# Kernel optimization log

Measured on AMD Instinct MI355X. Metric: run time of the kernel, lower is better.

Reference implementation:

```python
import jax, jax.numpy as jnp
import numpy as np

# neuralef_loss_cfg constants (kernel = '10nnn_sigm1.0')
T = 10.0        # cfg['t']
ALPHA = 0.05    # cfg['alpha']
KNN = 10        # parsed from '10nnn'
SIGMA2 = 1.0    # parsed from 'sigm1.0'
EPS = 1e-12     # F.normalize eps

N_TOKENS, D_FEAT, K_EIG = 8192, 768, 256


def setup_inputs() -> dict:
    key = jax.random.key(0)
    k1, k2 = jax.random.split(key)
    FF = jax.random.normal(k1, (N_TOKENS, D_FEAT), dtype=jnp.float32)
    Psi = jax.random.normal(k2, (N_TOKENS, K_EIG), dtype=jnp.float32)
    return {"FF": FF, "Psi": Psi}


def _gram_knn(FF):
    """torch.no_grad() block: RBF affinity -> topk KNN sparsify -> sym -> degree norm."""
    # input_l2_normalize: F.normalize(FF, dim=1)
    FFn = FF / jnp.maximum(jnp.linalg.norm(FF, axis=1, keepdims=True), EPS)
    sq = jnp.sum(FFn * FFn, axis=-1)                       # [N]
    # pairwise squared distances -> RBF kernel  [N, N]
    A = jnp.exp(-(sq[:, None] + sq[None, :] - 2.0 * (FFn @ FFn.T)) / (2.0 * SIGMA2))
    vals, idx = jax.lax.top_k(A, KNN)                      # [N, KNN]
    N = A.shape[0]
    rows = jnp.arange(N)
    # res.scatter_(1, idx, vals) on zeros_like(A)
    res = jnp.zeros_like(A).at[rows[:, None], idx].set(vals)
    gram = 0.5 * (res + res.T)
    gram = gram.at[rows, rows].set(0.0)                    # zero diagonal
    Dsum = jnp.sum(gram, axis=-1)
    # D = Dsum.rsqrt(); D[D==inf] = 0  (Dsum >= 0 always since vals >= 0)
    D = jnp.where(Dsum > 0, jax.lax.rsqrt(Dsum), 0.0)
    return D[:, None] * gram * D[None, :]


def reference(FF, Psi):
    N = Psi.shape[0]
    Psi = Psi * (T / N)
    gram = jax.lax.stop_gradient(_gram_knn(FF))            # [N, N]
    gPsi = gram @ Psi                                      # [N, K]
    R = Psi.T @ gPsi                                       # [K, K]
    # no_sg = False: R_hat = Psi.T.detach() @ gram @ Psi
    R_hat = jax.lax.stop_gradient(Psi).T @ gPsi
    loss = -jnp.trace(R)
    reg = jnp.sum(jnp.triu(R_hat ** 2, 1))
    return jnp.stack([loss, reg * ALPHA])
```

## Files before the change

### kernel.cpp

```cpp
#include <hip/hip_runtime.h>
#include <math.h>

#define N_TOK 8192
#define D_FEAT 768
#define K_EIG 256
#define KNN 10
#define CAP 256
#define NCHUNK 4
#define CHUNK 2048

typedef unsigned short ushort_t;
typedef float f32x4 __attribute__((ext_vector_type(4)));
typedef short bf16x8 __attribute__((ext_vector_type(8)));
typedef unsigned short u16x8 __attribute__((ext_vector_type(8)));
typedef unsigned short u16x4 __attribute__((ext_vector_type(4)));

__device__ inline float u2f(unsigned u) { union { unsigned u; float f; } c; c.u = u; return c.f; }
__device__ inline unsigned f2u(float f) { union { unsigned u; float f; } c; c.f = f; return c.u; }
__device__ inline ushort_t f2bf_rne(float f) {
  const unsigned u = f2u(f);
  return (ushort_t)((u + 0x7fffu + ((u >> 16) & 1u)) >> 16);
}
__device__ inline ushort_t f2key(float f) {
  const unsigned h = f2u(f) >> 16;
  return (ushort_t)((h & 0x8000u) ? (h ^ 0xFFFFu) : (h | 0x8000u));
}
__device__ inline float key2f(unsigned k) {
  const unsigned h = (k & 0x8000u) ? (k ^ 0x8000u) : (k ^ 0xFFFFu);
  return u2f(h << 16);
}
__device__ inline unsigned wave_max_u32(unsigned m) {
#pragma unroll
  for (int s = 1; s < 64; s <<= 1) m = max(m, (unsigned)__shfl_xor((int)m, s, 64));
  return m;
}

__global__ __launch_bounds__(192) void k_norm(const float* __restrict__ FF,
                                              ushort_t* __restrict__ FFbf,
                                              float* __restrict__ rn,
                                              float* __restrict__ sqv) {
  const int row = blockIdx.x;
  const int tid = threadIdx.x;
  const float4 v = *(const float4*)&FF[(size_t)row * D_FEAT + tid * 4];
  float s = v.x * v.x + v.y * v.y + v.z * v.z + v.w * v.w;
  __shared__ float red[3];
  for (int m = 32; m > 0; m >>= 1) s += __shfl_xor(s, m, 64);
  if ((tid & 63) == 0) red[tid >> 6] = s;
  __syncthreads();
  const float tot = red[0] + red[1] + red[2];
  const float scale = 1.f / fmaxf(sqrtf(tot), 1e-12f);
  float4 w;
  w.x = v.x * scale; w.y = v.y * scale; w.z = v.z * scale; w.w = v.w * scale;
  float s2 = w.x * w.x + w.y * w.y + w.z * w.z + w.w * w.w;
  u16x4 o;
  o[0] = f2bf_rne(w.x); o[1] = f2bf_rne(w.y); o[2] = f2bf_rne(w.z); o[3] = f2bf_rne(w.w);
  *(u16x4*)&FFbf[(size_t)row * D_FEAT + tid * 4] = o;
  for (int m = 32; m > 0; m >>= 1) s2 += __shfl_xor(s2, m, 64);
  __syncthreads();
  if ((tid & 63) == 0) red[tid >> 6] = s2;
  __syncthreads();
  if (tid == 0) { sqv[row] = red[0] + red[1] + red[2]; rn[row] = scale; }
}

#define AS1(p) ((const __attribute__((address_space(1))) void*)(p))
#define AS3(p) ((__attribute__((address_space(3))) void*)(p))

__global__ __launch_bounds__(256) void k_gemm(const ushort_t* __restrict__ FFbf,
                                              ushort_t* __restrict__ Cs,
                                              ushort_t* __restrict__ Gmax,
                                              int cbase) {
  __shared__ ushort_t smem[16384];
  const int tid = threadIdx.x;
  const int mb = blockIdx.x & 63;
  const int nb = blockIdx.x >> 6;
  const int rbase = mb * 128;
  const int cb = cbase + nb * 128;
  const int w = tid >> 6, lane = tid & 63;
  const int wr = w >> 1, wc = w & 1;
  const int fr = lane & 15;
  const int kg = lane >> 4;
  const int srow = tid >> 2, skq = tid & 3;

  f32x4 acc[4][4];
#pragma unroll
  for (int m = 0; m < 4; ++m)
#pragma unroll
    for (int n = 0; n < 4; ++n) acc[m][n] = (f32x4){0.f, 0.f, 0.f, 0.f};

#define STAGE(b, kt) do { \
    const ushort_t* ga = FFbf + (size_t)(rbase + srow) * D_FEAT + (kt) * 32 + skq * 8; \
    const ushort_t* gb = FFbf + (size_t)(cb + srow) * D_FEAT + (kt) * 32 + skq * 8; \
    char* abase = (char*)&smem[(b) * 4096]; \
    char* bbase = (char*)&smem[8192 + (b) * 4096]; \
    __builtin_amdgcn_global_load_lds(AS1(ga), AS3(abase + tid * 16), 16, 0, 0); \
    __builtin_amdgcn_global_load_lds(AS1(gb), AS3(bbase + tid * 16), 16, 0, 0); \
    __builtin_amdgcn_global_load_lds(AS1(ga + (size_t)64 * D_FEAT), AS3(abase + 4096 + tid * 16), 16, 0, 0); \
    __builtin_amdgcn_global_load_lds(AS1(gb + (size_t)64 * D_FEAT), AS3(bbase + 4096 + tid * 16), 16, 0, 0); \
  } while (0)

  STAGE(0, 0);
  int buf = 0;
  for (int kt = 0; kt < D_FEAT / 32; ++kt) {
    __syncthreads();
    if (kt + 1 < D_FEAT / 32) STAGE(buf ^ 1, kt + 1);
    bf16x8 af[4], bfr[4];
#pragma unroll
    for (int m = 0; m < 4; ++m)
      af[m] = *(const bf16x8*)&smem[buf * 4096 + (wr * 64 + m * 16 + fr) * 32 + kg * 8];
#pragma unroll
    for (int n = 0; n < 4; ++n)
      bfr[n] = *(const bf16x8*)&smem[8192 + buf * 4096 + (wc * 64 + n * 16 + fr) * 32 + kg * 8];
#pragma unroll
    for (int m = 0; m < 4; ++m)
#pragma unroll
      for (int n = 0; n < 4; ++n)
        acc[m][n] = __builtin_amdgcn_mfma_f32_16x16x32_bf16(af[m], bfr[n], acc[m][n], 0, 0, 0);
    buf ^= 1;
  }
#undef STAGE

  __syncthreads();
#pragma unroll
  for (int m = 0; m < 4; ++m)
#pragma unroll
    for (int n = 0; n < 4; ++n)
#pragma unroll
      for (int r = 0; r < 4; ++r)
        smem[(wr * 64 + m * 16 + kg * 4 + r) * 128 + wc * 64 + n * 16 + fr] = f2key(acc[m][n][r]);
  __syncthreads();
#pragma unroll
  for (int i = 0; i < 8; ++i) {
    const int off = i * 4096 + tid * 16;
    const int row = off >> 8;
    const int colb = off & 255;
    const u16x8 v = *(const u16x8*)((const char*)smem + off);
    *(u16x8*)((char*)Cs + (size_t)(rbase + row) * (CHUNK * 2) + (size_t)nb * 256 + colb) = v;
  }
  {
    const int r2 = tid >> 1;
    const int gh = (tid & 1) * 8;
    u16x8 gmv;
#pragma unroll
    for (int g = 0; g < 8; ++g) {
      const u16x8 grp = *(const u16x8*)&smem[r2 * 128 + (gh + g) * 8];
      unsigned mx = 0;
#pragma unroll
      for (int j = 0; j < 8; ++j) mx = max(mx, (unsigned)(ushort_t)grp[j]);
      gmv[g] = (ushort_t)mx;
    }
    *(u16x8*)&Gmax[(size_t)(rbase + r2) * 256 + nb * 16 + gh] = gmv;
  }
}

__global__ __launch_bounds__(256) void k_sel(const ushort_t* __restrict__ Cs,
                                             const ushort_t* __restrict__ Gmax,
                                             int chunk,
                                             float* __restrict__ pd, int* __restrict__ pi) {
  const int tid = threadIdx.x;
  const int lane = tid & 63;
  const int row = blockIdx.x * 4 + (tid >> 6);
  const ushort_t* src = Cs + (size_t)row * CHUNK;

  const u16x4 gm = *(const u16x4*)&Gmax[(size_t)row * 256 + lane * 4];
  unsigned cur[4];
#pragma unroll
  for (int k = 0; k < 4; ++k)
    cur[k] = (((unsigned)(ushort_t)gm[k]) << 16) | (unsigned)(lane * 4 + k);
  unsigned keep = 0;
#pragma unroll
  for (int r = 0; r < 16; ++r) {
    unsigned m = max(max(cur[0], cur[1]), max(cur[2], cur[3]));
    m = wave_max_u32(m);
    if (lane == r) keep = m;
    const unsigned gid = m & 0xFFu;
    if (lane == (int)(gid >> 2)) {
      const int sl = (int)(gid & 3u);
#pragma unroll
      for (int k = 0; k < 4; ++k)
        if (k == sl) cur[k] = 0;
    }
  }
  const unsigned gid2 = keep & 0xFFu;
  unsigned E[8];
  if (lane < 16) {
    const u16x8 g = *(const u16x8*)&src[gid2 * 8];
#pragma unroll
    for (int j = 0; j < 8; ++j)
      E[j] = (((unsigned)(ushort_t)g[j]) << 16) | (gid2 * 8 + (unsigned)j);
  } else {
#pragma unroll
    for (int j = 0; j < 8; ++j) E[j] = 0;
  }
  unsigned keep2 = 0;
#pragma unroll
  for (int r = 0; r < 16; ++r) {
    unsigned m = E[0];
#pragma unroll
    for (int j = 1; j < 8; ++j) m = max(m, E[j]);
    m = wave_max_u32(m);
    if (lane == r) keep2 = m;
    const unsigned col = m & 0xFFFFu;
    const bool mine = (lane < 16) && ((col >> 3) == gid2);
    const int sl = (int)(col & 7u);
#pragma unroll
    for (int j = 0; j < 8; ++j)
      if (mine && j == sl) E[j] = 0;
  }
  if (lane < 16) {
    pd[((size_t)row * NCHUNK + chunk) * 16 + lane] = key2f(keep2 >> 16);
    pi[((size_t)row * NCHUNK + chunk) * 16 + lane] = chunk * CHUNK + (int)(keep2 & 0xFFFFu);
  }
}

__global__ __launch_bounds__(256) void k_rescore(const float* __restrict__ FF,
                                                 const float* __restrict__ rn,
                                                 const float* __restrict__ sqv,
                                                 const float* __restrict__ pd,
                                                 const int* __restrict__ pi,
                                                 float* __restrict__ tv, int* __restrict__ tj) {
  const int tid = threadIdx.x;
  const int lane = tid & 63;
  const int row = blockIdx.x * 4 + (tid >> 6);

  const float pdv = pd[(size_t)row * 64 + lane];
  const int myj = pi[(size_t)row * 64 + lane];
  unsigned cur = (((unsigned)f2key(pdv)) << 16) | (unsigned)lane;
  int selj = 0;
#pragma unroll
  for (int r = 0; r < 16; ++r) {
    const unsigned m = wave_max_u32(cur);
    const int wln = (int)(m & 63u);
    const int jw = __shfl(myj, wln, 64);
    if (lane == r) selj = jw;
    if (lane == wln) cur = 0;
  }

  const float si = rn[row];
  const float sqi = sqv[row];
  const float* fi = FF + (size_t)row * D_FEAT;
  float4 a0 = *(const float4*)&fi[lane * 4];
  float4 a1 = *(const float4*)&fi[256 + lane * 4];
  float4 a2 = *(const float4*)&fi[512 + lane * 4];
  a0.x *= si; a0.y *= si; a0.z *= si; a0.w *= si;
  a1.x *= si; a1.y *= si; a1.z *= si; a1.w *= si;
  a2.x *= si; a2.y *= si; a2.z *= si; a2.w *= si;

  float dsc_l = 0.f, dvl_l = 0.f; int j_l = 0;
#pragma unroll 4
  for (int c = 0; c < 16; ++c) {
    const int j = __shfl(selj, c, 64);
    const float sj = rn[j];
    const float* fj = FF + (size_t)j * D_FEAT;
    const float4 b0 = *(const float4*)&fj[lane * 4];
    const float4 b1 = *(const float4*)&fj[256 + lane * 4];
    const float4 b2 = *(const float4*)&fj[512 + lane * 4];
    float acc = 0.f;
    acc = fmaf(a0.x, b0.x * sj, acc); acc = fmaf(a0.y, b0.y * sj, acc);
    acc = fmaf(a0.z, b0.z * sj, acc); acc = fmaf(a0.w, b0.w * sj, acc);
    acc = fmaf(a1.x, b1.x * sj, acc); acc = fmaf(a1.y, b1.y * sj, acc);
    acc = fmaf(a1.z, b1.z * sj, acc); acc = fmaf(a1.w, b1.w * sj, acc);
    acc = fmaf(a2.x, b2.x * sj, acc); acc = fmaf(a2.y, b2.y * sj, acc);
    acc = fmaf(a2.z, b2.z * sj, acc); acc = fmaf(a2.w, b2.w * sj, acc);
#pragma unroll
    for (int m = 32; m > 0; m >>= 1) acc += __shfl_xor(acc, m, 64);
    if (lane == c) {
      const float sqj = sqv[j];
      j_l = j;
      dsc_l = acc - 0.5f * sqj;
      dvl_l = expf(-0.5f * (sqi + sqj - 2.f * acc));
    }
  }

  unsigned fk = 0;
  if (lane < 16) {
    const unsigned u = f2u(dsc_l);
    fk = u ^ ((u >> 31) ? 0xFFFFFFFFu : 0x80000000u);
  }
#pragma unroll
  for (int s = 0; s < 10; ++s) {
    const unsigned m = wave_max_u32(fk);
    const unsigned long long bal = __ballot(fk == m);
    const int wln = __ffsll((unsigned long long)bal) - 1;
    const float tvv = __shfl(dvl_l, wln, 64);
    const int tjj = __shfl(j_l, wln, 64);
    if (lane == s) {
      tv[(size_t)row * KNN + s] = tvv;
      tj[(size_t)row * KNN + s] = tjj;
    }
    if (lane == wln) fk = 0;
  }
}

__global__ void k_scatter(const float* __restrict__ tv, const int* __restrict__ tj,
                          int* __restrict__ cnt, int* __restrict__ nbrJ,
                          float* __restrict__ nbrW) {
  const int e = blockIdx.x * blockDim.x + threadIdx.x;
  if (e >= N_TOK * KNN) return;
  const int i = e / KNN;
  const int j = tj[e];
  if (j == i) return;
  const float w = 0.5f * tv[e];
  const int p = atomicAdd(&cnt[i], 1);
  if (p < CAP) { nbrJ[(size_t)i * CAP + p] = j; nbrW[(size_t)i * CAP + p] = w; }
  const int q = atomicAdd(&cnt[j], 1);
  if (q < CAP) { nbrJ[(size_t)j * CAP + q] = i; nbrW[(size_t)j * CAP + q] = w; }
}

__global__ void k_degree(const int* __restrict__ cnt, const float* __restrict__ nbrW,
                         float* __restrict__ Dv) {
  const int r = blockIdx.x * 4 + (threadIdx.x >> 6);
  const int lane = threadIdx.x & 63;
  const int c = min(cnt[r], CAP);
  float s = 0.f;
  for (int m = lane; m < c; m += 64) s += nbrW[(size_t)r * CAP + m];
  for (int m = 32; m > 0; m >>= 1) s += __shfl_xor(s, m, 64);
  if (lane == 0) Dv[r] = (s > 0.f) ? rsqrtf(s) : 0.f;
}

__global__ __launch_bounds__(256) void k_gpsi(const float* __restrict__ Psi,
                                              const int* __restrict__ cnt,
                                              const int* __restrict__ nbrJ,
                                              const float* __restrict__ nbrW,
                                              const float* __restrict__ Dv,
                                              float* __restrict__ gP) {
  const int i = blockIdx.x;
  const int tid = threadIdx.x;
  __shared__ int sJ[CAP];
  __shared__ float sW[CAP];
  const int c = min(cnt[i], CAP);
  if (tid < c) {
    const int j = nbrJ[(size_t)i * CAP + tid];
    sJ[tid] = j;
    sW[tid] = nbrW[(size_t)i * CAP + tid] * Dv[j];
  }
  __syncthreads();
  float acc = 0.f;
  for (int m = 0; m < c; ++m) acc += sW[m] * Psi[(size_t)sJ[m] * K_EIG + tid];
  gP[(size_t)i * K_EIG + tid] = acc * Dv[i];
}

__global__ __launch_bounds__(256) void k_Rpart(const float* __restrict__ Psi,
                                               const float* __restrict__ gP,
                                               float* __restrict__ Rp) {
  __shared__ float sP[64][68];
  __shared__ float sG[64][68];
  const int tid = threadIdx.x;
  const int ks = blockIdx.x >> 4;
  const int tile = blockIdx.x & 15;
  const int at = (tile >> 2) * 64;
  const int bt = (tile & 3) * 64;
  const int a4 = (tid & 15) * 4;
  const int b4 = (tid >> 4) * 4;
  const int lr = tid >> 2;

  float acc[4][4];
#pragma unroll
  for (int i = 0; i < 4; ++i)
#pragma unroll
    for (int j = 0; j < 4; ++j) acc[i][j] = 0.f;

  for (int rt = 0; rt < 8; ++rt) {
    const int r0 = ks * 512 + rt * 64;
    __syncthreads();
#pragma unroll
    for (int q = 0; q < 4; ++q) {
      const int seg = (tid & 3) + q * 4;
      *(float4*)&sP[lr][seg * 4] = *(const float4*)&Psi[(size_t)(r0 + lr) * K_EIG + at + seg * 4];
      *(float4*)&sG[lr][seg * 4] = *(const float4*)&gP[(size_t)(r0 + lr) * K_EIG + bt + seg * 4];
    }
    __syncthreads();
#pragma unroll 4
    for (int r = 0; r < 64; ++r) {
      const float4 pa = *(const float4*)&sP[r][a4];
      const float4 pg = *(const float4*)&sG[r][b4];
      acc[0][0] = fmaf(pa.x, pg.x, acc[0][0]); acc[0][1] = fmaf(pa.x, pg.y, acc[0][1]);
      acc[0][2] = fmaf(pa.x, pg.z, acc[0][2]); acc[0][3] = fmaf(pa.x, pg.w, acc[0][3]);
      acc[1][0] = fmaf(pa.y, pg.x, acc[1][0]); acc[1][1] = fmaf(pa.y, pg.y, acc[1][1]);
      acc[1][2] = fmaf(pa.y, pg.z, acc[1][2]); acc[1][3] = fmaf(pa.y, pg.w, acc[1][3]);
      acc[2][0] = fmaf(pa.z, pg.x, acc[2][0]); acc[2][1] = fmaf(pa.z, pg.y, acc[2][1]);
      acc[2][2] = fmaf(pa.z, pg.z, acc[2][2]); acc[2][3] = fmaf(pa.z, pg.w, acc[2][3]);
      acc[3][0] = fmaf(pa.w, pg.x, acc[3][0]); acc[3][1] = fmaf(pa.w, pg.y, acc[3][1]);
      acc[3][2] = fmaf(pa.w, pg.z, acc[3][2]); acc[3][3] = fmaf(pa.w, pg.w, acc[3][3]);
    }
  }
#pragma unroll
  for (int i = 0; i < 4; ++i) {
    float4 o; o.x = acc[i][0]; o.y = acc[i][1]; o.z = acc[i][2]; o.w = acc[i][3];
    *(float4*)&Rp[(size_t)ks * (K_EIG * K_EIG) + (size_t)(at + a4 + i) * K_EIG + bt + b4] = o;
  }
}

__global__ __launch_bounds__(256) void k_Rred(const float* __restrict__ Rp,
                                              double* __restrict__ part) {
  const int tid = threadIdx.x;
  const int e0 = blockIdx.x * 1024 + tid * 4;
  float4 s = {0.f, 0.f, 0.f, 0.f};
  for (int ks = 0; ks < 16; ++ks) {
    const float4 v = *(const float4*)&Rp[(size_t)ks * (K_EIG * K_EIG) + e0];
    s.x += v.x; s.y += v.y; s.z += v.z; s.w += v.w;
  }
  const float sc = (10.f / 8192.f) * (10.f / 8192.f);
  double tl = 0.0, rg = 0.0;
#pragma unroll
  for (int j = 0; j < 4; ++j) {
    const int e = e0 + j;
    const int a = e >> 8, b = e & 255;
    const double v = (double)(((const float*)&s)[j] * sc);
    if (a == b) tl += v;
    else if (b > a) rg += v * v;
  }
  __shared__ double st[256], sr[256];
  st[tid] = tl; sr[tid] = rg;
  __syncthreads();
  for (int w = 128; w > 0; w >>= 1) {
    if (tid < w) { st[tid] += st[tid + w]; sr[tid] += sr[tid + w]; }
    __syncthreads();
  }
  if (tid == 0) { part[blockIdx.x] = st[0]; part[64 + blockIdx.x] = sr[0]; }
}

__global__ void k_final2(const double* __restrict__ part, float* __restrict__ out) {
  const int lane = threadIdx.x;
  double tl = part[lane];
  double rg = part[64 + lane];
  for (int m = 32; m > 0; m >>= 1) {
    tl += __shfl_xor(tl, m, 64);
    rg += __shfl_xor(rg, m, 64);
  }
  if (lane == 0) {
    out[0] = (float)(-tl);
    out[1] = (float)(rg * 0.05);
  }
}

extern "C" void kernel_launch(void* const* d_in, const int* in_sizes, int n_in,
                              void* d_out, int out_size, void* d_ws, size_t ws_size,
                              hipStream_t stream) {
  const float* FF = (const float*)d_in[0];
  const float* Psi = (const float*)d_in[1];
  float* out = (float*)d_out;
  float* ws = (float*)d_ws;

  size_t o = 0;
  ushort_t* FFbf = (ushort_t*)(ws + o); o += (size_t)N_TOK * D_FEAT / 2;
  float* rn  = ws + o; o += N_TOK;
  float* sqv = ws + o; o += N_TOK;
  float* pd  = ws + o; o += (size_t)N_TOK * NCHUNK * 16;
  int*   pi  = (int*)(ws + o); o += (size_t)N_TOK * NCHUNK * 16;
  float* tv  = ws + o; o += (size_t)N_TOK * KNN;
  int*   tj  = (int*)(ws + o); o += (size_t)N_TOK * KNN;
  int*   cnt = (int*)(ws + o); o += N_TOK;
  double* part = (double*)(ws + o); o += 256;
  ushort_t* Gmax = (ushort_t*)(ws + o); o += (size_t)N_TOK * 256 / 2;
  char* X = (char*)(ws + o);
  ushort_t* Cs = (ushort_t*)X;
  int*   nbrJ = (int*)X;
  float* nbrW = (float*)(X + (size_t)N_TOK * CAP * 4);
  float* Dv   = (float*)(X + 2 * (size_t)N_TOK * CAP * 4);
  float* gP   = (float*)(X + 2 * (size_t)N_TOK * CAP * 4 + (size_t)N_TOK * 4);
  float* Rp   = (float*)(X + 25ull * 1024 * 1024);

  k_norm<<<N_TOK, 192, 0, stream>>>(FF, FFbf, rn, sqv);
  for (int c = 0; c < NCHUNK; ++c) {
    k_gemm<<<(N_TOK / 128) * (CHUNK / 128), 256, 0, stream>>>(FFbf, Cs, Gmax, c * CHUNK);
    k_sel<<<N_TOK / 4, 256, 0, stream>>>(Cs, Gmax, c, pd, pi);
  }
  k_rescore<<<N_TOK / 4, 256, 0, stream>>>(FF, rn, sqv, pd, pi, tv, tj);
  hipMemsetAsync(cnt, 0, N_TOK * sizeof(int), stream);
  k_scatter<<<(N_TOK * KNN + 255) / 256, 256, 0, stream>>>(tv, tj, cnt, nbrJ, nbrW);
  k_degree<<<N_TOK / 4, 256, 0, stream>>>(cnt, nbrW, Dv);
  k_gpsi<<<N_TOK, 256, 0, stream>>>(Psi, cnt, nbrJ, nbrW, Dv, gP);
  k_Rpart<<<256, 256, 0, stream>>>(Psi, gP, Rp);
  k_Rred<<<64, 256, 0, stream>>>(Rp, part);
  k_final2<<<1, 64, 0, stream>>>(part, out);
}
```

Measured before the change: 392.5 us.

## Exploit Gram symmetry: compute only upper-triangular tiles and write transposed copies

The similarity GEMM is restructured into 2048x2048 super-blocks, and only the diagonal and upper-triangular blocks are computed. Each tile's keys are also written transposed, either into the same buffer (diagonal blocks) or into a separate CsT buffer, so both row sets can run top-k selection. The Gmax side buffer is removed and group maxima are recomputed inside k_sel from the stored keys. This roughly halves MFMA work, at the cost of more kernel launches (16 sel + 10 gemm), smaller grids (136 or 256 blocks), and uncoalesced transposed stores.

```diff
diff --git a/kernel.cpp b/kernel.cpp
--- a/kernel.cpp
+++ b/kernel.cpp
@@ -7,7 +7,7 @@
 #define KNN 10
 #define CAP 256
 #define NCHUNK 4
-#define CHUNK 2048
+#define SB 2048
 
 typedef unsigned short ushort_t;
 typedef float f32x4 __attribute__((ext_vector_type(4)));
@@ -65,16 +65,24 @@
 #define AS1(p) ((const __attribute__((address_space(1))) void*)(p))
 #define AS3(p) ((__attribute__((address_space(3))) void*)(p))
 
-__global__ __launch_bounds__(256) void k_gemm(const ushort_t* __restrict__ FFbf,
-                                              ushort_t* __restrict__ Cs,
-                                              ushort_t* __restrict__ Gmax,
-                                              int cbase) {
+__global__ __launch_bounds__(256) void k_gemm_sym(const ushort_t* __restrict__ FFbf,
+                                                  ushort_t* __restrict__ Cs,
+                                                  ushort_t* __restrict__ CsT,
+                                                  int rowBase, int colBase, int diag) {
   __shared__ ushort_t smem[16384];
   const int tid = threadIdx.x;
-  const int mb = blockIdx.x & 63;
-  const int nb = blockIdx.x >> 6;
-  const int rbase = mb * 128;
-  const int cb = cbase + nb * 128;
+  int mb, nb;
+  if (diag) {
+    const int t = blockIdx.x;
+    int rb = (int)((sqrtf(8.f * (float)t + 1.f) - 1.f) * 0.5f);
+    while ((rb + 1) * (rb + 2) / 2 <= t) ++rb;
+    while (rb * (rb + 1) / 2 > t) --rb;
+    mb = rb; nb = t - rb * (rb + 1) / 2;
+  } else {
+    mb = blockIdx.x >> 4; nb = blockIdx.x & 15;
+  }
+  const int aRow = rowBase + mb * 128;
+  const int bRow = colBase + nb * 128;
   const int w = tid >> 6, lane = tid & 63;
   const int wr = w >> 1, wc = w & 1;
   const int fr = lane & 15;
@@ -88,8 +96,8 @@
     for (int n = 0; n < 4; ++n) acc[m][n] = (f32x4){0.f, 0.f, 0.f, 0.f};
 
 #define STAGE(b, kt) do { \
-    const ushort_t* ga = FFbf + (size_t)(rbase + srow) * D_FEAT + (kt) * 32 + skq * 8; \
-    const ushort_t* gb = FFbf + (size_t)(cb + srow) * D_FEAT + (kt) * 32 + skq * 8; \
+    const ushort_t* ga = FFbf + (size_t)(aRow + srow) * D_FEAT + (kt) * 32 + skq * 8; \
+    const ushort_t* gb = FFbf + (size_t)(bRow + srow) * D_FEAT + (kt) * 32 + skq * 8; \
     char* abase = (char*)&smem[(b) * 4096]; \
     char* bbase = (char*)&smem[8192 + (b) * 4096]; \
     __builtin_amdgcn_global_load_lds(AS1(ga), AS3(abase + tid * 16), 16, 0, 0); \
@@ -127,6 +135,22 @@
 #pragma unroll
       for (int r = 0; r < 4; ++r)
         smem[(wr * 64 + m * 16 + kg * 4 + r) * 128 + wc * 64 + n * 16 + fr] = f2key(acc[m][n][r]);
+
+  if (!diag || mb != nb) {
+    ushort_t* T = diag ? Cs : CsT;
+#pragma unroll
+    for (int m = 0; m < 4; ++m) {
+#pragma unroll
+      for (int n = 0; n < 4; ++n) {
+        u16x4 k4;
+#pragma unroll
+        for (int r = 0; r < 4; ++r) k4[r] = f2key(acc[m][n][r]);
+        const int cl = nb * 128 + wc * 64 + n * 16 + fr;
+        const int rl0 = mb * 128 + wr * 64 + m * 16 + kg * 4;
+        *(u16x4*)&T[(size_t)cl * SB + rl0] = k4;
+      }
+    }
+  }
   __syncthreads();
 #pragma unroll
   for (int i = 0; i < 8; ++i) {
@@ -134,51 +158,38 @@
     const int row = off >> 8;
     const int colb = off & 255;
     const u16x8 v = *(const u16x8*)((const char*)smem + off);
-    *(u16x8*)((char*)Cs + (size_t)(rbase + row) * (CHUNK * 2) + (size_t)nb * 256 + colb) = v;
-  }
-  {
-    const int r2 = tid >> 1;
-    const int gh = (tid & 1) * 8;
-    u16x8 gmv;
-#pragma unroll
-    for (int g = 0; g < 8; ++g) {
-      const u16x8 grp = *(const u16x8*)&smem[r2 * 128 + (gh + g) * 8];
-      unsigned mx = 0;
-#pragma unroll
-      for (int j = 0; j < 8; ++j) mx = max(mx, (unsigned)(ushort_t)grp[j]);
-      gmv[g] = (ushort_t)mx;
-    }
-    *(u16x8*)&Gmax[(size_t)(rbase + r2) * 256 + nb * 16 + gh] = gmv;
-  }
-}
-
-__global__ __launch_bounds__(256) void k_sel(const ushort_t* __restrict__ Cs,
-                                             const ushort_t* __restrict__ Gmax,
-                                             int chunk,
+    *(u16x8*)((char*)Cs + (size_t)(mb * 128 + row) * (SB * 2) + (size_t)nb * 256 + colb) = v;
+  }
+}
+
+__global__ __launch_bounds__(256) void k_sel(const ushort_t* __restrict__ CsBuf,
+                                             int rowBase, int colBase, int colChunk,
                                              float* __restrict__ pd, int* __restrict__ pi) {
   const int tid = threadIdx.x;
   const int lane = tid & 63;
-  const int row = blockIdx.x * 4 + (tid >> 6);
-  const ushort_t* src = Cs + (size_t)row * CHUNK;
-
-  const u16x4 gm = *(const u16x4*)&Gmax[(size_t)row * 256 + lane * 4];
-  unsigned cur[4];
-#pragma unroll
-  for (int k = 0; k < 4; ++k)
-    cur[k] = (((unsigned)(ushort_t)gm[k]) << 16) | (unsigned)(lane * 4 + k);
+  const int rl = blockIdx.x * 4 + (tid >> 6);
+  const ushort_t* src = CsBuf + (size_t)rl * SB;
+
+  unsigned G[4];
+#pragma unroll
+  for (int t = 0; t < 4; ++t) {
+    const u16x8 raw = *(const u16x8*)&src[t * 512 + lane * 8];
+    unsigned m = 0;
+#pragma unroll
+    for (int j = 0; j < 8; ++j) m = max(m, (unsigned)(ushort_t)raw[j]);
+    G[t] = (m << 16) | (unsigned)(t * 64 + lane);
+  }
   unsigned keep = 0;
 #pragma unroll
   for (int r = 0; r < 16; ++r) {
-    unsigned m = max(max(cur[0], cur[1]), max(cur[2], cur[3]));
+    unsigned m = max(max(G[0], G[1]), max(G[2], G[3]));
     m = wave_max_u32(m);
     if (lane == r) keep = m;
     const unsigned gid = m & 0xFFu;
-    if (lane == (int)(gid >> 2)) {
-      const int sl = (int)(gid & 3u);
-#pragma unroll
-      for (int k = 0; k < 4; ++k)
-        if (k == sl) cur[k] = 0;
-    }
+    const int ow = (int)(gid & 63u), sl = (int)(gid >> 6);
+#pragma unroll
+    for (int t = 0; t < 4; ++t)
+      if (lane == ow && t == sl) G[t] = 0;
   }
   const unsigned gid2 = keep & 0xFFu;
   unsigned E[8];
@@ -207,8 +218,9 @@
       if (mine && j == sl) E[j] = 0;
   }
   if (lane < 16) {
-    pd[((size_t)row * NCHUNK + chunk) * 16 + lane] = key2f(keep2 >> 16);
-    pi[((size_t)row * NCHUNK + chunk) * 16 + lane] = chunk * CHUNK + (int)(keep2 & 0xFFFFu);
+    const int grow = rowBase + rl;
+    pd[((size_t)grow * NCHUNK + colChunk) * 16 + lane] = key2f(keep2 >> 16);
+    pi[((size_t)grow * NCHUNK + colChunk) * 16 + lane] = colBase + (int)(keep2 & 0xFFFFu);
   }
 }
 
@@ -451,9 +463,9 @@
   int*   tj  = (int*)(ws + o); o += (size_t)N_TOK * KNN;
   int*   cnt = (int*)(ws + o); o += N_TOK;
   double* part = (double*)(ws + o); o += 256;
-  ushort_t* Gmax = (ushort_t*)(ws + o); o += (size_t)N_TOK * 256 / 2;
   char* X = (char*)(ws + o);
-  ushort_t* Cs = (ushort_t*)X;
+  ushort_t* Cs  = (ushort_t*)X;
+  ushort_t* CsT = (ushort_t*)(X + (size_t)SB * SB * 2);
   int*   nbrJ = (int*)X;
   float* nbrW = (float*)(X + (size_t)N_TOK * CAP * 4);
   float* Dv   = (float*)(X + 2 * (size_t)N_TOK * CAP * 4);
@@ -461,9 +473,14 @@
   float* Rp   = (float*)(X + 25ull * 1024 * 1024);
 
   k_norm<<<N_TOK, 192, 0, stream>>>(FF, FFbf, rn, sqv);
-  for (int c = 0; c < NCHUNK; ++c) {
-    k_gemm<<<(N_TOK / 128) * (CHUNK / 128), 256, 0, stream>>>(FFbf, Cs, Gmax, c * CHUNK);
-    k_sel<<<N_TOK / 4, 256, 0, stream>>>(Cs, Gmax, c, pd, pi);
+  for (int a = 0; a < 4; ++a) {
+    k_gemm_sym<<<136, 256, 0, stream>>>(FFbf, Cs, Cs, a * SB, a * SB, 1);
+    k_sel<<<SB / 4, 256, 0, stream>>>(Cs, a * SB, a * SB, a, pd, pi);
+    for (int b = a + 1; b < 4; ++b) {
+      k_gemm_sym<<<256, 256, 0, stream>>>(FFbf, Cs, CsT, a * SB, b * SB, 0);
+      k_sel<<<SB / 4, 256, 0, stream>>>(Cs, a * SB, b * SB, b, pd, pi);
+      k_sel<<<SB / 4, 256, 0, stream>>>(CsT, b * SB, a * SB, a, pd, pi);
+    }
   }
   k_rescore<<<N_TOK / 4, 256, 0, stream>>>(FF, rn, sqv, pd, pi, tv, tj);
   hipMemsetAsync(cnt, 0, N_TOK * sizeof(int), stream);
```

After: 504.2 us. 1.28x slower.
